# Performance work log

Measured on AMD Instinct MI355X. Metric: run time of the kernel, lower is better.

Reference implementation:

```python
import jax, jax.numpy as jnp
import numpy as np

D_MODEL = 1024
NUM_HEADS = 16
HEAD_DIM = D_MODEL // NUM_HEADS


def setup_inputs() -> dict:
    key = jax.random.key(0)
    k_x, k_wqkv, k_bqkv, k_wfc, k_bfc = jax.random.split(key, 5)
    scale_in = 1.0 / np.sqrt(D_MODEL)
    return {
        "x": jax.random.normal(k_x, (2, 2048, D_MODEL), dtype=jnp.float32),
        # torch nn.Linear stores weight as [out_features, in_features]
        "w_qkv": jax.random.uniform(k_wqkv, (3 * D_MODEL, D_MODEL), jnp.float32, -scale_in, scale_in),
        "b_qkv": jax.random.uniform(k_bqkv, (3 * D_MODEL,), jnp.float32, -scale_in, scale_in),
        "w_fc": jax.random.uniform(k_wfc, (D_MODEL, D_MODEL), jnp.float32, -scale_in, scale_in),
        "b_fc": jax.random.uniform(k_bfc, (D_MODEL,), jnp.float32, -scale_in, scale_in),
    }


def reference(x, w_qkv, b_qkv, w_fc, b_fc):
    B, S, _ = x.shape
    # fused QKV projection: [B,S,3*d_model]
    qkv = jnp.einsum("bsd,ed->bse", x, w_qkv) + b_qkv
    # [B,S,H,3*head_dim] -> [B,H,S,3*head_dim]
    qkv = qkv.reshape(B, S, NUM_HEADS, 3 * HEAD_DIM).transpose(0, 2, 1, 3)
    Q, K, V = jnp.split(qkv, 3, axis=-1)  # each [B,H,S,head_dim]
    scores = jnp.einsum("bhqd,bhkd->bhqk", Q, K) / np.sqrt(HEAD_DIM).astype(np.float32)
    attention = jax.nn.softmax(scores, axis=-1)  # [B,H,S,S]
    values = jnp.einsum("bhqk,bhkd->bhqd", attention, V)
    # [B,H,S,head_dim] -> [B,S,d_model]
    values = values.transpose(0, 2, 1, 3).reshape(B, S, D_MODEL)
    out = jnp.einsum("bsd,ed->bse", values, w_fc) + b_fc
    return out
```

## Files before the change

### kernel.cpp

```cpp
#include <hip/hip_runtime.h>
#include <hip/hip_bf16.h>
#include <hip/hip_fp16.h>

#define D_MODEL 1024
#define NH 16
#define HD 64
#define BATCH 2
#define SEQ 2048

typedef __attribute__((ext_vector_type(8))) short short8;
typedef __attribute__((ext_vector_type(4))) float floatx4;
typedef __attribute__((ext_vector_type(8))) _Float16 half8;

static __device__ __forceinline__ short f2bf(float f) {
    __hip_bfloat16 h = __float2bfloat16(f);
    return *reinterpret_cast<short*>(&h);
}
static __device__ __forceinline__ unsigned int pk2bf(float a, float b) {
    float2 t; t.x = a; t.y = b;
    __hip_bfloat162 h2 = __float22bfloat162_rn(t);
    return *reinterpret_cast<unsigned int*>(&h2);
}

__global__ __launch_bounds__(256) void cvt_all(
    const float* __restrict__ x, const float* __restrict__ wq,
    const float* __restrict__ wf,
    short* __restrict__ Xb, short* __restrict__ Wqb, short* __restrict__ Wfb)
{
    int i = blockIdx.x * 256 + threadIdx.x;
    const float* src; short* dst; int off;
    if (i < 524288)      { src = x;  dst = Xb;  off = i; }
    else if (i < 917504) { src = wq; dst = Wqb; off = i - 524288; }
    else                 { src = wf; dst = Wfb; off = i - 917504; }
    float4 a = *reinterpret_cast<const float4*>(src + off * 8);
    float4 b = *reinterpret_cast<const float4*>(src + off * 8 + 4);
    short8 o;
    o[0] = f2bf(a.x); o[1] = f2bf(a.y); o[2] = f2bf(a.z); o[3] = f2bf(a.w);
    o[4] = f2bf(b.x); o[5] = f2bf(b.y); o[6] = f2bf(b.z); o[7] = f2bf(b.w);
    *reinterpret_cast<short8*>(dst + off * 8) = o;
}

__global__ __launch_bounds__(256) void qkv_gemm(
    const short* __restrict__ X, const short* __restrict__ W,
    const float* __restrict__ bias,
    short* __restrict__ Qs, short* __restrict__ Ks, short* __restrict__ Vt_g)
{
    __shared__ __align__(16) short As[128][72];
    __shared__ __align__(16) short Bs[128][72];
    const int tid = threadIdx.x;
    const int m0 = blockIdx.y * 128;
    const int n0 = blockIdx.x * 128;
    const int bi = m0 >> 11, sl0 = m0 & 2047;
    const int w = tid >> 6, lane = tid & 63;
    const int quad = lane >> 4, l15 = lane & 15;
    const int wm2 = w >> 1, wn2 = w & 1;

    floatx4 acc[4][4];
#pragma unroll
    for (int i = 0; i < 4; i++)
#pragma unroll
        for (int j = 0; j < 4; j++) acc[i][j] = (floatx4)0.0f;

    for (int k0 = 0; k0 < 1024; k0 += 64) {
        __syncthreads();
#pragma unroll
        for (int i = 0; i < 4; i++) {
            int c = tid + i * 256;
            int row = c >> 3, ck = c & 7;
            *reinterpret_cast<uint4*>(&As[row][ck * 8]) =
                *reinterpret_cast<const uint4*>(&X[(m0 + row) * 1024 + k0 + ck * 8]);
            *reinterpret_cast<uint4*>(&Bs[row][ck * 8]) =
                *reinterpret_cast<const uint4*>(&W[(n0 + row) * 1024 + k0 + ck * 8]);
        }
        __syncthreads();
#pragma unroll
        for (int kk = 0; kk < 2; kk++) {
            short8 a[4], b[4];
#pragma unroll
            for (int t = 0; t < 4; t++) {
                a[t] = *reinterpret_cast<const short8*>(&As[wm2 * 64 + t * 16 + l15][kk * 32 + quad * 8]);
                b[t] = *reinterpret_cast<const short8*>(&Bs[wn2 * 64 + t * 16 + l15][kk * 32 + quad * 8]);
            }
#pragma unroll
            for (int mt = 0; mt < 4; mt++)
#pragma unroll
                for (int nt = 0; nt < 4; nt++)
                    acc[mt][nt] = __builtin_amdgcn_mfma_f32_16x16x32_bf16(
                        a[mt], b[nt], acc[mt][nt], 0, 0, 0);
        }
    }

    __syncthreads();
    short* T = &As[0][0];
#pragma unroll
    for (int half = 0; half < 2; half++) {
        const int colg0 = n0 + half * 64;
        const int h = colg0 / 192;
        const int t = (colg0 % 192) / 64;
        if (wn2 == half) {
#pragma unroll
            for (int nt = 0; nt < 4; nt++) {
                int jj = nt * 16 + l15;
                float bv = bias[colg0 + jj];
#pragma unroll
                for (int mt = 0; mt < 4; mt++) {
#pragma unroll
                    for (int r = 0; r < 4; r++) {
                        int ml = wm2 * 64 + mt * 16 + quad * 4 + r;
                        float v = acc[mt][nt][r] + bv;
                        if (t == 0) v *= 0.18033688f;
                        if (t < 2) As[ml][jj] = f2bf(v);
                        else       T[jj * 136 + ml] = f2bf(v);
                    }
                }
            }
        }
        __syncthreads();
        if (t < 2) {
            short* dst = (t == 0) ? Qs : Ks;
#pragma unroll
            for (int i = 0; i < 4; i++) {
                int c = tid + i * 256;
                int row = c >> 3, ck = c & 7;
                uint4 u = *reinterpret_cast<const uint4*>(&As[row][ck * 8]);
                *reinterpret_cast<uint4*>(
                    &dst[((size_t)(bi * NH + h) * SEQ + sl0 + row) * HD + ck * 8]) = u;
            }
        } else {
#pragma unroll
            for (int i = 0; i < 4; i++) {
                int c = tid + i * 256;
                int d = c >> 4, ck = c & 15;
                uint4 u = *reinterpret_cast<const uint4*>(&T[d * 136 + ck * 8]);
                *reinterpret_cast<uint4*>(
                    &Vt_g[((size_t)(bi * NH + h) * HD + d) * SEQ + sl0 + ck * 8]) = u;
            }
        }
        __syncthreads();
    }
}

__global__ __launch_bounds__(256, 4) void attn_kernel(
    const short* __restrict__ Qs, const short* __restrict__ Ks,
    const short* __restrict__ Vt_g,
    _Float16* __restrict__ Opart, float* __restrict__ lpart)
{
    __shared__ __align__(16) short Kl[64][72];
    __shared__ __align__(16) short Vt[64][72];
    __shared__ __align__(16) short Pl[4][32][72];

    const int tid = threadIdx.x;
    const int w = tid >> 6, lane = tid & 63;
    const int quad = lane >> 4, l15 = lane & 15;
    const int bx = blockIdx.x;
    const int khalf = bx & 1;
    const int q0 = (bx >> 1) * 128;
    const int h = blockIdx.y, bi = blockIdx.z;
    const int bh = bi * NH + h;
    const int kbase = bh * SEQ * HD;
    const int vbase = bh * HD * SEQ;
    const int kt0 = khalf * (SEQ / 2);

    const int kr0 = tid >> 3,         kc0 = (tid & 7) * 8;
    const int kr1 = (tid + 256) >> 3, kc1 = (tid & 7) * 8;

    const short8 onesv = {(short)0x3F80, (short)0x3F80, (short)0x3F80, (short)0x3F80,
                          (short)0x3F80, (short)0x3F80, (short)0x3F80, (short)0x3F80};

    short8 aq[2][2];
#pragma unroll
    for (int qt2 = 0; qt2 < 2; qt2++) {
        const short* qp = Qs + kbase + (q0 + w * 32 + qt2 * 16 + l15) * HD;
#pragma unroll
        for (int c = 0; c < 2; c++)
            aq[qt2][c] = *reinterpret_cast<const short8*>(qp + c * 32 + quad * 8);
    }

    floatx4 o[2][4], ol[2];
#pragma unroll
    for (int mt = 0; mt < 2; mt++) {
        ol[mt] = (floatx4)0.0f;
#pragma unroll
        for (int nt = 0; nt < 4; nt++) o[mt][nt] = (floatx4)0.0f;
    }

    for (int it = 0; it < SEQ / 128; it++) {
        const int kt = kt0 + it * 64;
        __syncthreads();
        *reinterpret_cast<uint4*>(&Kl[kr0][kc0]) =
            *reinterpret_cast<const uint4*>(&Ks[kbase + (kt + kr0) * HD + kc0]);
        *reinterpret_cast<uint4*>(&Kl[kr1][kc1]) =
            *reinterpret_cast<const uint4*>(&Ks[kbase + (kt + kr1) * HD + kc1]);
        *reinterpret_cast<uint4*>(&Vt[kr0][kc0]) =
            *reinterpret_cast<const uint4*>(&Vt_g[vbase + kr0 * SEQ + kt + kc0]);
        *reinterpret_cast<uint4*>(&Vt[kr1][kc1]) =
            *reinterpret_cast<const uint4*>(&Vt_g[vbase + kr1 * SEQ + kt + kc1]);
        __syncthreads();

        floatx4 sf[4][2];
#pragma unroll
        for (int kt2 = 0; kt2 < 4; kt2++)
#pragma unroll
            for (int qt2 = 0; qt2 < 2; qt2++) sf[kt2][qt2] = (floatx4)0.0f;
#pragma unroll
        for (int c = 0; c < 2; c++) {
#pragma unroll
            for (int kt2 = 0; kt2 < 4; kt2++) {
                short8 bk = *reinterpret_cast<const short8*>(
                    &Kl[kt2 * 16 + l15][c * 32 + quad * 8]);
#pragma unroll
                for (int qt2 = 0; qt2 < 2; qt2++)
                    sf[kt2][qt2] = __builtin_amdgcn_mfma_f32_16x16x32_bf16(
                        bk, aq[qt2][c], sf[kt2][qt2], 0, 0, 0);
            }
        }

#pragma unroll
        for (int kt2 = 0; kt2 < 4; kt2++) {
#pragma unroll
            for (int qt2 = 0; qt2 < 2; qt2++) {
                uint2 p;
                p.x = pk2bf(exp2f(sf[kt2][qt2][0]), exp2f(sf[kt2][qt2][1]));
                p.y = pk2bf(exp2f(sf[kt2][qt2][2]), exp2f(sf[kt2][qt2][3]));
                *reinterpret_cast<uint2*>(&Pl[w][qt2 * 16 + l15][kt2 * 16 + quad * 4]) = p;
            }
        }
        asm volatile("s_waitcnt lgkmcnt(0)" ::: "memory");

#pragma unroll
        for (int c = 0; c < 2; c++) {
            short8 vf[4];
#pragma unroll
            for (int nt = 0; nt < 4; nt++)
                vf[nt] = *reinterpret_cast<const short8*>(
                    &Vt[nt * 16 + l15][c * 32 + quad * 8]);
#pragma unroll
            for (int mt = 0; mt < 2; mt++) {
                short8 ap = *reinterpret_cast<const short8*>(
                    &Pl[w][mt * 16 + l15][c * 32 + quad * 8]);
#pragma unroll
                for (int nt = 0; nt < 4; nt++)
                    o[mt][nt] = __builtin_amdgcn_mfma_f32_16x16x32_bf16(
                        ap, vf[nt], o[mt][nt], 0, 0, 0);
                ol[mt] = __builtin_amdgcn_mfma_f32_16x16x32_bf16(
                    ap, onesv, ol[mt], 0, 0, 0);
            }
        }
    }

#pragma unroll
    for (int mt = 0; mt < 2; mt++) {
#pragma unroll
        for (int r = 0; r < 4; r++) {
            int ql = q0 + w * 32 + mt * 16 + quad * 4 + r;
            size_t base = (size_t)khalf * (4096u * 1024u) +
                          ((size_t)bi * SEQ + ql) * D_MODEL + h * HD;
#pragma unroll
            for (int nt = 0; nt < 4; nt++)
                Opart[base + nt * 16 + l15] = (_Float16)o[mt][nt][r];
            if (l15 == 0)
                lpart[khalf * 65536 + bh * SEQ + ql] = ol[mt][r];
        }
    }
}

__global__ __launch_bounds__(256) void combine_kernel(
    const _Float16* __restrict__ O, const float* __restrict__ lp,
    short* __restrict__ attnb)
{
    int i = blockIdx.x * 256 + threadIdx.x;
    int m = i >> 7;
    int e0 = (i & 127) * 8;
    int bi = m >> 11, s = m & 2047, h = e0 >> 6;
    int bh = bi * NH + h;
    float l = lp[bh * SEQ + s] + lp[65536 + bh * SEQ + s];
    float rl = 1.0f / l;
    size_t off = (size_t)m * D_MODEL + e0;
    half8 a = *reinterpret_cast<const half8*>(O + off);
    half8 b = *reinterpret_cast<const half8*>(O + 4096u * 1024u + off);
    short8 out;
#pragma unroll
    for (int j = 0; j < 8; j++)
        out[j] = f2bf(((float)a[j] + (float)b[j]) * rl);
    *reinterpret_cast<short8*>(attnb + off) = out;
}

__global__ __launch_bounds__(256) void fc_gemm(
    const short* __restrict__ A, const short* __restrict__ W,
    const float* __restrict__ bias, float* __restrict__ out)
{
    __shared__ __align__(16) short As[128][72];
    __shared__ __align__(16) short Bs[64][72];
    const int tid = threadIdx.x;
    const int m0 = blockIdx.y * 128;
    const int n0 = blockIdx.x * 64;
    const int w = tid >> 6, lane = tid & 63;
    const int quad = lane >> 4, l15 = lane & 15;
    const int wm2 = w >> 1, wn2 = w & 1;

    floatx4 acc[4][2];
#pragma unroll
    for (int i = 0; i < 4; i++)
#pragma unroll
        for (int j = 0; j < 2; j++) acc[i][j] = (floatx4)0.0f;

    for (int k0 = 0; k0 < 1024; k0 += 64) {
        __syncthreads();
#pragma unroll
        for (int i = 0; i < 4; i++) {
            int c = tid + i * 256;
            int row = c >> 3, ck = c & 7;
            *reinterpret_cast<uint4*>(&As[row][ck * 8]) =
                *reinterpret_cast<const uint4*>(&A[(m0 + row) * 1024 + k0 + ck * 8]);
        }
#pragma unroll
        for (int i = 0; i < 2; i++) {
            int c = tid + i * 256;
            int row = c >> 3, ck = c & 7;
            *reinterpret_cast<uint4*>(&Bs[row][ck * 8]) =
                *reinterpret_cast<const uint4*>(&W[(n0 + row) * 1024 + k0 + ck * 8]);
        }
        __syncthreads();
#pragma unroll
        for (int kk = 0; kk < 2; kk++) {
            short8 a[4], b[2];
#pragma unroll
            for (int i = 0; i < 4; i++)
                a[i] = *reinterpret_cast<const short8*>(&As[wm2 * 64 + i * 16 + l15][kk * 32 + quad * 8]);
#pragma unroll
            for (int j = 0; j < 2; j++)
                b[j] = *reinterpret_cast<const short8*>(&Bs[wn2 * 32 + j * 16 + l15][kk * 32 + quad * 8]);
#pragma unroll
            for (int mt = 0; mt < 4; mt++)
#pragma unroll
                for (int nt = 0; nt < 2; nt++)
                    acc[mt][nt] = __builtin_amdgcn_mfma_f32_16x16x32_bf16(
                        a[mt], b[nt], acc[mt][nt], 0, 0, 0);
        }
    }

#pragma unroll
    for (int nt = 0; nt < 2; nt++) {
        int col = n0 + wn2 * 32 + nt * 16 + l15;
        float bv = bias[col];
#pragma unroll
        for (int mt = 0; mt < 4; mt++) {
#pragma unroll
            for (int r = 0; r < 4; r++) {
                int row = m0 + wm2 * 64 + mt * 16 + quad * 4 + r;
                out[row * 1024 + col] = acc[mt][nt][r] + bv;
            }
        }
    }
}

extern "C" void kernel_launch(void* const* d_in, const int* in_sizes, int n_in,
                              void* d_out, int out_size, void* d_ws, size_t ws_size,
                              hipStream_t stream) {
    const float* x     = (const float*)d_in[0];
    const float* w_qkv = (const float*)d_in[1];
    const float* b_qkv = (const float*)d_in[2];
    const float* w_fc  = (const float*)d_in[3];
    const float* b_fc  = (const float*)d_in[4];
    float* out = (float*)d_out;

    const size_t M1 = 1024u * 1024u;
    short* ws = (short*)d_ws;
    short* Qs    = ws;
    short* Ks    = ws + 4 * M1;
    short* Vt_g  = ws + 8 * M1;
    short* Wfb   = ws + 12 * M1;
    short* Xb    = ws + 13 * M1;
    short* Wqb   = ws + 17 * M1;
    _Float16* Opart = (_Float16*)(ws + 13 * M1);
    float* lpart = (float*)(ws + 21 * M1);
    short* attnb = Qs;

    cvt_all<<<4096, 256, 0, stream>>>(x, w_qkv, w_fc, Xb, Wqb, Wfb);
    qkv_gemm<<<dim3(24, 32), 256, 0, stream>>>(Xb, Wqb, b_qkv, Qs, Ks, Vt_g);
    attn_kernel<<<dim3(32, 16, 2), 256, 0, stream>>>(Qs, Ks, Vt_g, Opart, lpart);
    combine_kernel<<<2048, 256, 0, stream>>>(Opart, lpart, attnb);
    fc_gemm<<<dim3(16, 32), 256, 0, stream>>>(attnb, Wfb, b_fc, out);
}
```

Before: 222.3 us.

## Split attention keys four ways with atomic fp32 accumulation and smaller tiles

Splits each query block's key range into four chunks instead of two, doubling the attention grid. Partial outputs and row sums are accumulated into fp32 buffers with atomicAdd, replacing separate fp16 partials, and a new zero-fill kernel clears those buffers first. The key tile shrinks to 32 and the launch bound targets 8 blocks per CU, aiming at higher occupancy and more parallelism. The cost is atomic traffic, an extra launch, and fp32 read bandwidth in the combine step.

```diff
diff --git a/kernel.cpp b/kernel.cpp
--- a/kernel.cpp
+++ b/kernel.cpp
@@ -1,6 +1,5 @@
 #include <hip/hip_runtime.h>
 #include <hip/hip_bf16.h>
-#include <hip/hip_fp16.h>
 
 #define D_MODEL 1024
 #define NH 16
@@ -10,7 +9,6 @@
 
 typedef __attribute__((ext_vector_type(8))) short short8;
 typedef __attribute__((ext_vector_type(4))) float floatx4;
-typedef __attribute__((ext_vector_type(8))) _Float16 half8;
 
 static __device__ __forceinline__ short f2bf(float f) {
     __hip_bfloat16 h = __float2bfloat16(f);
@@ -40,6 +38,12 @@
     *reinterpret_cast<short8*>(dst + off * 8) = o;
 }
 
+__global__ __launch_bounds__(256) void zero_fill(float* __restrict__ p)
+{
+    int i = blockIdx.x * 256 + threadIdx.x;
+    *reinterpret_cast<float4*>(p + (size_t)i * 4) = float4{0.f, 0.f, 0.f, 0.f};
+}
+
 __global__ __launch_bounds__(256) void qkv_gemm(
     const short* __restrict__ X, const short* __restrict__ W,
     const float* __restrict__ bias,
@@ -140,29 +144,28 @@
     }
 }
 
-__global__ __launch_bounds__(256, 4) void attn_kernel(
+__global__ __launch_bounds__(256, 8) void attn_kernel(
     const short* __restrict__ Qs, const short* __restrict__ Ks,
     const short* __restrict__ Vt_g,
-    _Float16* __restrict__ Opart, float* __restrict__ lpart)
-{
-    __shared__ __align__(16) short Kl[64][72];
-    __shared__ __align__(16) short Vt[64][72];
-    __shared__ __align__(16) short Pl[4][32][72];
+    float* __restrict__ Oacc, float* __restrict__ lacc)
+{
+    __shared__ __align__(16) short Kl[32][72];
+    __shared__ __align__(16) short Vt[64][40];
+    __shared__ __align__(16) short Pl[4][32][40];
 
     const int tid = threadIdx.x;
     const int w = tid >> 6, lane = tid & 63;
     const int quad = lane >> 4, l15 = lane & 15;
     const int bx = blockIdx.x;
-    const int khalf = bx & 1;
-    const int q0 = (bx >> 1) * 128;
+    const int q0 = (bx >> 2) * 128;
+    const int kt0 = (bx & 3) * (SEQ / 4);
     const int h = blockIdx.y, bi = blockIdx.z;
     const int bh = bi * NH + h;
     const int kbase = bh * SEQ * HD;
     const int vbase = bh * HD * SEQ;
-    const int kt0 = khalf * (SEQ / 2);
-
-    const int kr0 = tid >> 3,         kc0 = (tid & 7) * 8;
-    const int kr1 = (tid + 256) >> 3, kc1 = (tid & 7) * 8;
+
+    const int krow = tid >> 3, kck = (tid & 7) * 8;
+    const int vd = tid >> 2,   vkc = (tid & 3) * 8;
 
     const short8 onesv = {(short)0x3F80, (short)0x3F80, (short)0x3F80, (short)0x3F80,
                           (short)0x3F80, (short)0x3F80, (short)0x3F80, (short)0x3F80};
@@ -184,28 +187,24 @@
         for (int nt = 0; nt < 4; nt++) o[mt][nt] = (floatx4)0.0f;
     }
 
-    for (int it = 0; it < SEQ / 128; it++) {
-        const int kt = kt0 + it * 64;
-        __syncthreads();
-        *reinterpret_cast<uint4*>(&Kl[kr0][kc0]) =
-            *reinterpret_cast<const uint4*>(&Ks[kbase + (kt + kr0) * HD + kc0]);
-        *reinterpret_cast<uint4*>(&Kl[kr1][kc1]) =
-            *reinterpret_cast<const uint4*>(&Ks[kbase + (kt + kr1) * HD + kc1]);
-        *reinterpret_cast<uint4*>(&Vt[kr0][kc0]) =
-            *reinterpret_cast<const uint4*>(&Vt_g[vbase + kr0 * SEQ + kt + kc0]);
-        *reinterpret_cast<uint4*>(&Vt[kr1][kc1]) =
-            *reinterpret_cast<const uint4*>(&Vt_g[vbase + kr1 * SEQ + kt + kc1]);
-        __syncthreads();
-
-        floatx4 sf[4][2];
-#pragma unroll
-        for (int kt2 = 0; kt2 < 4; kt2++)
+    for (int it = 0; it < SEQ / 4 / 32; it++) {
+        const int kt = kt0 + it * 32;
+        __syncthreads();
+        *reinterpret_cast<uint4*>(&Kl[krow][kck]) =
+            *reinterpret_cast<const uint4*>(&Ks[kbase + (kt + krow) * HD + kck]);
+        *reinterpret_cast<uint4*>(&Vt[vd][vkc]) =
+            *reinterpret_cast<const uint4*>(&Vt_g[vbase + vd * SEQ + kt + vkc]);
+        __syncthreads();
+
+        floatx4 sf[2][2];
+#pragma unroll
+        for (int kt2 = 0; kt2 < 2; kt2++)
 #pragma unroll
             for (int qt2 = 0; qt2 < 2; qt2++) sf[kt2][qt2] = (floatx4)0.0f;
 #pragma unroll
         for (int c = 0; c < 2; c++) {
 #pragma unroll
-            for (int kt2 = 0; kt2 < 4; kt2++) {
+            for (int kt2 = 0; kt2 < 2; kt2++) {
                 short8 bk = *reinterpret_cast<const short8*>(
                     &Kl[kt2 * 16 + l15][c * 32 + quad * 8]);
 #pragma unroll
@@ -216,7 +215,7 @@
         }
 
 #pragma unroll
-        for (int kt2 = 0; kt2 < 4; kt2++) {
+        for (int kt2 = 0; kt2 < 2; kt2++) {
 #pragma unroll
             for (int qt2 = 0; qt2 < 2; qt2++) {
                 uint2 p;
@@ -228,23 +227,16 @@
         asm volatile("s_waitcnt lgkmcnt(0)" ::: "memory");
 
 #pragma unroll
-        for (int c = 0; c < 2; c++) {
-            short8 vf[4];
-#pragma unroll
-            for (int nt = 0; nt < 4; nt++)
-                vf[nt] = *reinterpret_cast<const short8*>(
-                    &Vt[nt * 16 + l15][c * 32 + quad * 8]);
-#pragma unroll
-            for (int mt = 0; mt < 2; mt++) {
-                short8 ap = *reinterpret_cast<const short8*>(
-                    &Pl[w][mt * 16 + l15][c * 32 + quad * 8]);
-#pragma unroll
-                for (int nt = 0; nt < 4; nt++)
-                    o[mt][nt] = __builtin_amdgcn_mfma_f32_16x16x32_bf16(
-                        ap, vf[nt], o[mt][nt], 0, 0, 0);
-                ol[mt] = __builtin_amdgcn_mfma_f32_16x16x32_bf16(
-                    ap, onesv, ol[mt], 0, 0, 0);
-            }
+        for (int mt = 0; mt < 2; mt++) {
+            short8 ap = *reinterpret_cast<const short8*>(&Pl[w][mt * 16 + l15][quad * 8]);
+#pragma unroll
+            for (int nt = 0; nt < 4; nt++) {
+                short8 bv = *reinterpret_cast<const short8*>(&Vt[nt * 16 + l15][quad * 8]);
+                o[mt][nt] = __builtin_amdgcn_mfma_f32_16x16x32_bf16(
+                    ap, bv, o[mt][nt], 0, 0, 0);
+            }
+            ol[mt] = __builtin_amdgcn_mfma_f32_16x16x32_bf16(
+                ap, onesv, ol[mt], 0, 0, 0);
         }
     }
 
@@ -253,35 +245,33 @@
 #pragma unroll
         for (int r = 0; r < 4; r++) {
             int ql = q0 + w * 32 + mt * 16 + quad * 4 + r;
-            size_t base = (size_t)khalf * (4096u * 1024u) +
-                          ((size_t)bi * SEQ + ql) * D_MODEL + h * HD;
+            float* op = Oacc + ((size_t)bi * SEQ + ql) * D_MODEL + h * HD;
 #pragma unroll
             for (int nt = 0; nt < 4; nt++)
-                Opart[base + nt * 16 + l15] = (_Float16)o[mt][nt][r];
+                atomicAdd(op + nt * 16 + l15, o[mt][nt][r]);
             if (l15 == 0)
-                lpart[khalf * 65536 + bh * SEQ + ql] = ol[mt][r];
+                atomicAdd(lacc + bh * SEQ + ql, ol[mt][r]);
         }
     }
 }
 
 __global__ __launch_bounds__(256) void combine_kernel(
-    const _Float16* __restrict__ O, const float* __restrict__ lp,
+    const float* __restrict__ Oacc, const float* __restrict__ lacc,
     short* __restrict__ attnb)
 {
     int i = blockIdx.x * 256 + threadIdx.x;
     int m = i >> 7;
     int e0 = (i & 127) * 8;
     int bi = m >> 11, s = m & 2047, h = e0 >> 6;
-    int bh = bi * NH + h;
-    float l = lp[bh * SEQ + s] + lp[65536 + bh * SEQ + s];
-    float rl = 1.0f / l;
+    float rl = 1.0f / lacc[(bi * NH + h) * SEQ + s];
     size_t off = (size_t)m * D_MODEL + e0;
-    half8 a = *reinterpret_cast<const half8*>(O + off);
-    half8 b = *reinterpret_cast<const half8*>(O + 4096u * 1024u + off);
+    float4 a = *reinterpret_cast<const float4*>(Oacc + off);
+    float4 b = *reinterpret_cast<const float4*>(Oacc + off + 4);
     short8 out;
-#pragma unroll
-    for (int j = 0; j < 8; j++)
-        out[j] = f2bf(((float)a[j] + (float)b[j]) * rl);
+    out[0] = f2bf(a.x * rl); out[1] = f2bf(a.y * rl);
+    out[2] = f2bf(a.z * rl); out[3] = f2bf(a.w * rl);
+    out[4] = f2bf(b.x * rl); out[5] = f2bf(b.y * rl);
+    out[6] = f2bf(b.z * rl); out[7] = f2bf(b.w * rl);
     *reinterpret_cast<short8*>(attnb + off) = out;
 }
 
@@ -372,13 +362,14 @@
     short* Wfb   = ws + 12 * M1;
     short* Xb    = ws + 13 * M1;
     short* Wqb   = ws + 17 * M1;
-    _Float16* Opart = (_Float16*)(ws + 13 * M1);
-    float* lpart = (float*)(ws + 21 * M1);
+    float* Oacc  = (float*)(ws + 13 * M1);
+    float* lacc  = (float*)(ws + 21 * M1);
     short* attnb = Qs;
 
     cvt_all<<<4096, 256, 0, stream>>>(x, w_qkv, w_fc, Xb, Wqb, Wfb);
     qkv_gemm<<<dim3(24, 32), 256, 0, stream>>>(Xb, Wqb, b_qkv, Qs, Ks, Vt_g);
-    attn_kernel<<<dim3(32, 16, 2), 256, 0, stream>>>(Qs, Ks, Vt_g, Opart, lpart);
-    combine_kernel<<<2048, 256, 0, stream>>>(Opart, lpart, attnb);
+    zero_fill<<<4160, 256, 0, stream>>>(Oacc);
+    attn_kernel<<<dim3(64, 16, 2), 256, 0, stream>>>(Qs, Ks, Vt_g, Oacc, lacc);
+    combine_kernel<<<2048, 256, 0, stream>>>(Oacc, lacc, attnb);
     fc_gemm<<<dim3(16, 32), 256, 0, stream>>>(attnb, Wfb, b_fc, out);
 }
```

Result: slower. 429.2 us (+93.0%).
